# Performance work log

Measured on AMD Instinct MI355X. Metric: run time of the kernel, lower is better.

The kernel has to match this reference:

```python
import jax, jax.numpy as jnp
import numpy as np
from jax import lax

PRE_NMS_TOPN = 6000
POST_NMS_TOPN = 300
NMS_IOU = 0.7
VARIANCES = np.array([0.1, 0.1, 0.2, 0.2], dtype=np.float32)


def setup_inputs() -> dict:
    key = jax.random.key(0)
    k1, k2, k3, k4 = jax.random.split(key, 4)
    B, FH, FW, K = 32, 128, 128, 9
    A = FH * FW * K  # 147456 total anchors
    rpn_bbox_deltas = jax.random.normal(k1, (B, A, 4), dtype=jnp.float32) * 0.1
    rpn_labels = jax.random.normal(k2, (B, FH, FW, K), dtype=jnp.float32)
    # Anchors in [y1, x1, y2, x2] with y1<y2, x1<x2 on a ~1024px image.
    ctr = jax.random.uniform(k3, (A, 2), dtype=jnp.float32) * 1024.0
    wh = jax.random.uniform(k4, (A, 2), dtype=jnp.float32) * 224.0 + 32.0
    anchors = jnp.concatenate([ctr - 0.5 * wh, ctr + 0.5 * wh], axis=-1)
    return {"rpn_bbox_deltas": rpn_bbox_deltas, "rpn_labels": rpn_labels, "anchors": anchors}


def get_bboxes_from_deltas(anchors, deltas):
    # anchors: [A, 4] (y1,x1,y2,x2); deltas: [B, A, 4] (dy,dx,dh,dw)
    anc_w = anchors[..., 3] - anchors[..., 1]
    anc_h = anchors[..., 2] - anchors[..., 0]
    anc_cx = anchors[..., 1] + 0.5 * anc_w
    anc_cy = anchors[..., 0] + 0.5 * anc_h
    bb_w = jnp.exp(deltas[..., 3]) * anc_w
    bb_h = jnp.exp(deltas[..., 2]) * anc_h
    bb_cx = deltas[..., 1] * anc_w + anc_cx
    bb_cy = deltas[..., 0] * anc_h + anc_cy
    y1 = bb_cy - 0.5 * bb_h
    x1 = bb_cx - 0.5 * bb_w
    y2 = bb_h + y1
    x2 = bb_w + x1
    return jnp.stack([y1, x1, y2, x2], axis=-1)


def nms_per_image(boxes, scores, iou_threshold, num_keep):
    # boxes: [N, 4] sorted by descending score; scores: [N]
    y1, x1, y2, x2 = boxes[:, 0], boxes[:, 1], boxes[:, 2], boxes[:, 3]
    areas = (y2 - y1) * (x2 - x1)

    def step(scores_rem, _):
        idx = jnp.argmax(scores_rem)
        valid = jnp.isfinite(scores_rem[idx])
        b = boxes[idx]
        iy1 = jnp.maximum(b[0], y1)
        ix1 = jnp.maximum(b[1], x1)
        iy2 = jnp.minimum(b[2], y2)
        ix2 = jnp.minimum(b[3], x2)
        inter = jnp.clip(iy2 - iy1, 0.0) * jnp.clip(ix2 - ix1, 0.0)
        b_area = (b[2] - b[0]) * (b[3] - b[1])
        iou = inter / (areas + b_area - inter + 1e-9)
        # IoU(box, itself) == 1 > threshold, so the picked box is also suppressed.
        new_scores = jnp.where(iou > iou_threshold, -jnp.inf, scores_rem)
        return new_scores, (idx, valid)

    _, (keep_idx, valid) = lax.scan(step, scores, None, length=num_keep)
    vf = valid.astype(boxes.dtype)
    keep_boxes = boxes[keep_idx] * vf[:, None]  # zero-pad invalid slots
    keep_scores = scores[keep_idx] * vf
    return keep_boxes, keep_scores


def reference(rpn_bbox_deltas, rpn_labels, anchors):
    A = anchors.shape[0]
    B = rpn_bbox_deltas.shape[0]
    deltas = rpn_bbox_deltas.reshape(B, A, 4) * jnp.asarray(VARIANCES)
    labels = jax.nn.softmax(rpn_labels, axis=-1).reshape(B, A)
    rpn_bboxes = get_bboxes_from_deltas(anchors, deltas)  # [B, A, 4]
    # top-k pre-NMS filter (lax.top_k output is already sorted descending)
    pre_scores, pre_idx = lax.top_k(labels, PRE_NMS_TOPN)  # [B, P]
    pre_boxes = jnp.take_along_axis(rpn_bboxes, pre_idx[..., None], axis=1)  # [B, P, 4]
    nms_fn = lambda b, s: nms_per_image(b, s, NMS_IOU, POST_NMS_TOPN)
    roi_bboxes, roi_scores = jax.vmap(nms_fn)(pre_boxes, pre_scores)
    return roi_bboxes, roi_scores
```

## Files before the change

### kernel.cpp

```cpp
#include <hip/hip_runtime.h>
#include <cstdint>
#include <cstddef>

#pragma clang fp contract(off)

#define KCLS 9
#define PRE_N 6000
#define POST_N 300
#define NMS_IOU_T 0.7f
#define HIST_BLOCK 256
#define CHUNKS_PER_IMG 32
#define NMS_BLOCK 512
#define PICK_BLOCK 256
#define NSEG 4
#define SEG_CAP 4096

#define SUPP(pb, pa, mbx, mar, out) \
    bool out; { \
        float iy1_ = fmaxf((pb).x, (mbx).x); \
        float ix1_ = fmaxf((pb).y, (mbx).y); \
        float iy2_ = fminf((pb).z, (mbx).z); \
        float ix2_ = fminf((pb).w, (mbx).w); \
        float ih_ = iy2_ - iy1_; ih_ = ih_ > 0.f ? ih_ : 0.f; \
        float iw_ = ix2_ - ix1_; iw_ = iw_ > 0.f ? iw_ : 0.f; \
        float inter_ = ih_ * iw_; \
        float den_ = (mar) + (pa) - inter_ + 1e-9f; \
        float hi_ = 0.7000007f * den_; \
        float lo_ = 0.6999993f * den_; \
        out = inter_ > hi_; \
        if (inter_ >= lo_ && inter_ <= hi_) out = (inter_ / den_) > NMS_IOU_T; \
    }

__global__ void __launch_bounds__(256)
softmax_hist_kernel(const float* __restrict__ labels,
                    float* __restrict__ scores,
                    unsigned int* __restrict__ ghist,
                    int ngroups, int gpi) {
    __shared__ unsigned int h[2048];
    const int tid = threadIdx.x;
    for (int i = tid; i < 2048; i += 256) h[i] = 0u;
    __syncthreads();
    const int g = blockIdx.x * 256 + tid;
    if (g < ngroups) {
        const float* x = labels + (size_t)g * KCLS;
        float v[KCLS];
        float m = -1e30f;
        #pragma unroll
        for (int k = 0; k < KCLS; ++k) { v[k] = x[k]; m = fmaxf(m, v[k]); }
        float e[KCLS];
        float s = 0.f;
        #pragma unroll
        for (int k = 0; k < KCLS; ++k) { e[k] = expf(v[k] - m); s += e[k]; }
        float* o = scores + (size_t)g * KCLS;
        #pragma unroll
        for (int k = 0; k < KCLS; ++k) {
            float r = e[k] / s;
            o[k] = r;
            atomicAdd(&h[(__float_as_uint(r) >> 21) & 2047u], 1u);
        }
    }
    __syncthreads();
    const int img0 = (blockIdx.x * 256) / gpi;
    unsigned int* gh = ghist + (size_t)img0 * 2048;
    for (int i = tid; i < 2048; i += 256) {
        unsigned int c = h[i];
        if (c) atomicAdd(&gh[i], c);
    }
}

__global__ void hist_kernel(const float* __restrict__ scores,
                            unsigned int* __restrict__ ghist,
                            const unsigned int* __restrict__ state,
                            int A, int shift, int bins, unsigned int pmask) {
    __shared__ unsigned int h[2048];
    const int img = blockIdx.y;
    const int chunk = blockIdx.x;
    const int tid = threadIdx.x;
    for (int i = tid; i < bins; i += HIST_BLOCK) h[i] = 0u;
    __syncthreads();
    unsigned int prefix = pmask ? (state[img * 2 + 0] & pmask) : 0u;
    const int per = A / CHUNKS_PER_IMG;
    const float* sc = scores + (size_t)img * A + (size_t)chunk * per;
    for (int i = tid; i < per; i += HIST_BLOCK) {
        unsigned int v = __float_as_uint(sc[i]);
        if ((v & pmask) == prefix)
            atomicAdd(&h[(v >> shift) & (unsigned)(bins - 1)], 1u);
    }
    __syncthreads();
    unsigned int* gh = ghist + (size_t)img * 2048;
    for (int i = tid; i < bins; i += HIST_BLOCK) {
        unsigned int c = h[i];
        if (c) atomicAdd(&gh[i], c);
    }
}

__global__ void __launch_bounds__(PICK_BLOCK)
pick_kernel(const unsigned int* __restrict__ ghist,
            unsigned int* __restrict__ state,
            int shift, int bins, int first_pass) {
    const int img = blockIdx.x;
    const int t = threadIdx.x;
    const unsigned int* gh = ghist + (size_t)img * 2048;
    __shared__ unsigned int cnt[2048];
    __shared__ unsigned int ssum[PICK_BLOCK];
    const int per = bins / PICK_BLOCK;
    unsigned int my = 0;
    for (int i = 0; i < per; ++i) {
        unsigned int c = gh[t * per + i];
        cnt[t * per + i] = c;
        my += c;
    }
    ssum[t] = my;
    __syncthreads();
    for (int d = 1; d < PICK_BLOCK; d <<= 1) {
        unsigned int v = (t + d < PICK_BLOCK) ? ssum[t + d] : 0u;
        __syncthreads();
        ssum[t] += v;
        __syncthreads();
    }
    unsigned int prefix = first_pass ? 0u : state[img * 2 + 0];
    unsigned int krem = first_pass ? (unsigned)PRE_N : state[img * 2 + 1];
    unsigned int above = ssum[t] - my;
    if (above < krem && ssum[t] >= krem) {
        unsigned int cum = above;
        for (int b = per - 1; b >= 0; --b) {
            unsigned int c = cnt[t * per + b];
            if (cum + c >= krem) {
                state[img * 2 + 0] = prefix | ((unsigned int)(t * per + b) << shift);
                state[img * 2 + 1] = krem - cum;
                break;
            }
            cum += c;
        }
    }
}

#define CE(a, b, u) { if ((v[a] > v[b]) == (u)) { unsigned long long t_ = v[a]; v[a] = v[b]; v[b] = t_; } }
#define REG3(u) { CE(0,4,u) CE(1,5,u) CE(2,6,u) CE(3,7,u) \
                  CE(0,2,u) CE(1,3,u) CE(4,6,u) CE(5,7,u) \
                  CE(0,1,u) CE(2,3,u) CE(4,5,u) CE(6,7,u) }

__global__ void __launch_bounds__(512)
compact_sort_kernel(const float* __restrict__ scores,
                    const unsigned int* __restrict__ state,
                    unsigned long long* __restrict__ pool,
                    unsigned int* __restrict__ counts,
                    int A) {
    __shared__ unsigned long long lin[SEG_CAP];
    __shared__ unsigned int plo[2][SEG_CAP];
    __shared__ unsigned int phi[2][SEG_CAP];
    __shared__ unsigned int cnt;
    const int img = blockIdx.y;
    const int seg = blockIdx.x;
    const int tid = threadIdx.x;
    const int lane = tid & 63;
    const int w = tid >> 6;
    const float* sc = scores + (size_t)img * A;
    const unsigned int T = state[img * 2 + 0];

    if (tid == 0) cnt = 0u;
    for (int i = tid; i < SEG_CAP; i += 512) lin[i] = ~0ull;
    __syncthreads();

    const int ngr = A >> 6;
    const int nj = ngr / NSEG;
    for (int j = w; j < nj; j += 8) {
        int g = seg + j * NSEG;
        int i = (g << 6) + lane;
        unsigned int sv = __float_as_uint(sc[i]);
        bool push = (sv >= T);
        unsigned long long bal = __ballot(push ? 1 : 0);
        if (push) {
            int leader = __ffsll(bal) - 1;
            int rank = __popcll(bal & ((1ull << lane) - 1ull));
            unsigned int base = 0;
            if (lane == leader) base = atomicAdd(&cnt, (unsigned int)__popcll(bal));
            base = (unsigned int)__shfl((int)base, leader);
            unsigned int pos = base + (unsigned int)rank;
            if (pos < SEG_CAP)
                lin[pos] = (((unsigned long long)(~sv)) << 32) | (unsigned long long)(unsigned int)i;
        }
    }
    __syncthreads();

    int n = (int)cnt; if (n > SEG_CAP) n = SEG_CAP;
    int P2 = 512; while (P2 < n) P2 <<= 1;
    const int NT = P2 >> 3;
    const int t = tid;
    const bool act = (t < NT);

    unsigned long long v[8];
    if (act) {
        #pragma unroll
        for (int e = 0; e < 8; ++e) v[e] = lin[(t << 3) + e];
        CE(0,1,true) CE(2,3,false) CE(4,5,true) CE(6,7,false)
        CE(0,2,true) CE(1,3,true) CE(4,6,false) CE(5,7,false)
        CE(0,1,true) CE(2,3,true) CE(4,5,false) CE(6,7,false)
        bool u8 = ((t & 1) == 0);
        REG3(u8)
    }
    int b = 0;
    for (int k = 16; k <= P2; k <<= 1) {
        const bool up = (((t << 3) & k) == 0);
        for (int j = k >> 1; j >= 8; j >>= 1) {
            const int c = j >> 3;
            if (act) {
                #pragma unroll
                for (int e = 0; e < 8; ++e) {
                    int idx = e * NT + t;
                    plo[b][idx] = (unsigned int)v[e];
                    phi[b][idx] = (unsigned int)(v[e] >> 32);
                }
            }
            __syncthreads();
            if (act) {
                const int q = t ^ c;
                const bool keep_min = (up == ((t & c) == 0));
                #pragma unroll
                for (int e = 0; e < 8; ++e) {
                    int idx = e * NT + q;
                    unsigned long long wv = ((unsigned long long)phi[b][idx] << 32)
                                          | (unsigned long long)plo[b][idx];
                    bool less = v[e] < wv;
                    v[e] = (less == keep_min) ? v[e] : wv;
                }
            }
            b ^= 1;
        }
        if (act) { REG3(up) }
    }

    unsigned long long* gp = pool + ((size_t)img * NSEG + seg) * SEG_CAP;
    if (act) {
        #pragma unroll
        for (int e = 0; e < 8; ++e) {
            int r = (t << 3) + e;
            if (r < n) gp[r] = v[e];
        }
    }
    if (tid == 0) counts[img * NSEG + seg] = (unsigned int)n;
}

__global__ void __launch_bounds__(256)
rank_decode_kernel(const unsigned long long* __restrict__ pool,
                   const unsigned int* __restrict__ counts,
                   const float* __restrict__ deltas,
                   const float* __restrict__ anchors,
                   float* __restrict__ pre_boxes,
                   float* __restrict__ pre_scores,
                   int A) {
    __shared__ unsigned long long arr[2 * SEG_CAP];
    const int img = blockIdx.y;
    const int seg = blockIdx.x;
    const int tid = threadIdx.x;

    int c[NSEG], off[NSEG + 1];
    const unsigned long long* gp[NSEG];
    off[0] = 0;
    #pragma unroll
    for (int s = 0; s < NSEG; ++s) {
        int cs = (int)counts[img * NSEG + s];
        if (cs > SEG_CAP) cs = SEG_CAP;
        c[s] = cs;
        off[s + 1] = off[s] + cs;
        gp[s] = pool + ((size_t)img * NSEG + s) * SEG_CAP;
    }
    const int total = off[NSEG];
    const bool inlds = (total <= 2 * SEG_CAP);
    if (inlds) {
        #pragma unroll
        for (int s = 0; s < NSEG; ++s)
            for (int i = tid; i < c[s]; i += 256) arr[off[s] + i] = gp[s][i];
    }
    __syncthreads();

    const int m = c[seg];
    for (int i = tid; i < m; i += 256) {
        unsigned long long key = inlds ? arr[off[seg] + i] : gp[seg][i];
        int pos = i;
        #pragma unroll
        for (int s = 0; s < NSEG; ++s) {
            if (s == seg) continue;
            const unsigned long long* base = inlds ? (arr + off[s]) : gp[s];
            int lo = 0, hi = c[s];
            while (lo < hi) {
                int mid = (lo + hi) >> 1;
                if (base[mid] < key) lo = mid + 1; else hi = mid;
            }
            pos += lo;
        }
        if (pos < PRE_N) {
            unsigned int bidx = (unsigned int)(key & 0xFFFFFFFFull);
            unsigned int sbits = ~((unsigned int)(key >> 32));
            float score = __uint_as_float(sbits);
            float a0 = anchors[(size_t)bidx * 4 + 0];
            float a1 = anchors[(size_t)bidx * 4 + 1];
            float a2 = anchors[(size_t)bidx * 4 + 2];
            float a3 = anchors[(size_t)bidx * 4 + 3];
            const float* dd = deltas + ((size_t)img * A + bidx) * 4;
            float d0 = dd[0] * 0.1f;
            float d1 = dd[1] * 0.1f;
            float d2 = dd[2] * 0.2f;
            float d3 = dd[3] * 0.2f;
            float anc_w = a3 - a1;
            float anc_h = a2 - a0;
            float anc_cx = a1 + 0.5f * anc_w;
            float anc_cy = a0 + 0.5f * anc_h;
            float bb_w = expf(d3) * anc_w;
            float bb_h = expf(d2) * anc_h;
            float bb_cx = d1 * anc_w + anc_cx;
            float bb_cy = d0 * anc_h + anc_cy;
            float y1 = bb_cy - 0.5f * bb_h;
            float x1 = bb_cx - 0.5f * bb_w;
            float y2 = bb_h + y1;
            float x2 = bb_w + x1;
            float* ob = pre_boxes + ((size_t)img * PRE_N + pos) * 4;
            ob[0] = y1; ob[1] = x1; ob[2] = y2; ob[3] = x2;
            pre_scores[(size_t)img * PRE_N + pos] = score;
        }
    }
}

__global__ void __launch_bounds__(NMS_BLOCK)
nms_kernel(const float* __restrict__ pre_boxes,
           const float* __restrict__ pre_scores,
           float* __restrict__ out_boxes,
           float* __restrict__ out_scores) {
    const int img = blockIdx.x;
    const int tid = threadIdx.x;
    const int lane = tid & 63;
    const int grp = tid >> 6;
    const float4* bb4 = (const float4*)(pre_boxes + (size_t)img * PRE_N * 4);

    __shared__ float4 kept[POST_N];
    __shared__ float  kept_area[POST_N];
    __shared__ int    kept_idx[POST_N];
    __shared__ float4 chunkbox[64];
    __shared__ unsigned long long part[8][64];
    __shared__ unsigned long long supcol[64];
    __shared__ unsigned long long chunk_alive;
    __shared__ int kept_cnt;

    if (tid == 0) kept_cnt = 0;

    const int NCH = (PRE_N + 63) >> 6;

    float4 nb = make_float4(0.f, 0.f, 0.f, 0.f);
    if (grp == 0) nb = bb4[lane];

    for (int c = 0; c < NCH; ++c) {
        const int base = c << 6;
        if (grp == 0) chunkbox[lane] = nb;
        if (tid == 0) {
            int rem = PRE_N - base;
            chunk_alive = (rem >= 64) ? ~0ull : ((1ull << rem) - 1ull);
        }
        __syncthreads();

        if (grp == 0 && c + 1 < NCH) {
            int j = base + 64 + lane;
            nb = (j < PRE_N) ? bb4[j] : make_float4(0.f, 0.f, 0.f, 0.f);
        }

        const int K = kept_cnt;
        float4 mb = chunkbox[lane];
        float marea = (mb.z - mb.x) * (mb.w - mb.y);

        bool sup = false;
        for (int k = grp; k < K; k += 8) {
            float4 pb = kept[k];
            float pa = kept_area[k];
            SUPP(pb, pa, mb, marea, s)
            if (s) { sup = true; break; }
        }
        unsigned long long bal = __ballot(sup ? 1 : 0);
        if (lane == 0 && bal) atomicAnd(&chunk_alive, ~bal);

        unsigned long long pm = 0ull;
        #pragma unroll
        for (int u = 0; u < 8; ++u) {
            const int i = (grp << 3) + u;
            float4 pb = chunkbox[i];
            float pa = (pb.z - pb.x) * (pb.w - pb.y);
            SUPP(pb, pa, mb, marea, s)
            if (s) pm |= (1ull << i);
        }
        part[grp][lane] = pm;
        __syncthreads();

        if (grp == 0) {
            unsigned long long col = part[0][lane] | part[1][lane] | part[2][lane] | part[3][lane]
                                   | part[4][lane] | part[5][lane] | part[6][lane] | part[7][lane];
            supcol[lane] = col;
            const unsigned long long extm = chunk_alive;
            unsigned long long aliveset = 0ull;
            int kc = K;
            #pragma unroll 8
            for (int i = 0; i < 64; ++i) {
                unsigned long long mi = supcol[i];
                bool keep = (((extm >> i) & 1ull) != 0ull) &&
                            ((mi & aliveset) == 0ull) && (kc < POST_N);
                if (keep) {
                    if (lane == i) {
                        kept[kc] = mb;
                        kept_area[kc] = marea;
                        kept_idx[kc] = base + i;
                    }
                    aliveset |= (1ull << i);
                    ++kc;
                }
            }
            if (lane == 0) kept_cnt = kc;
        }
        __syncthreads();
        if (kept_cnt >= POST_N) break;
    }

    const int kc = kept_cnt;
    for (int r = tid; r < kc; r += NMS_BLOCK) {
        float4 bx = kept[r];
        float* ob = out_boxes + ((size_t)img * POST_N + r) * 4;
        ob[0] = bx.x; ob[1] = bx.y; ob[2] = bx.z; ob[3] = bx.w;
        out_scores[(size_t)img * POST_N + r] =
            pre_scores[(size_t)img * PRE_N + kept_idx[r]];
    }
}

extern "C" void kernel_launch(void* const* d_in, const int* in_sizes, int n_in,
                              void* d_out, int out_size, void* d_ws, size_t ws_size,
                              hipStream_t stream) {
    const float* deltas  = (const float*)d_in[0];
    const float* labels  = (const float*)d_in[1];
    const float* anchors = (const float*)d_in[2];
    float* out = (float*)d_out;

    const int A = in_sizes[2] / 4;
    const int B = in_sizes[0] / (A * 4);
    const int ngroups = in_sizes[1] / KCLS;
    const int gpi = ngroups / B;

    float* scores     = (float*)d_ws;
    float* pre_boxes  = scores + (size_t)B * A;
    float* pre_scores = pre_boxes + (size_t)B * PRE_N * 4;
    unsigned int* hist  = (unsigned int*)(pre_scores + (size_t)B * PRE_N);
    unsigned int* state = hist + (size_t)3 * B * 2048;
    unsigned long long* pool = (unsigned long long*)(state + (size_t)B * 2);
    unsigned int* counts = (unsigned int*)(pool + (size_t)B * NSEG * SEG_CAP);

    float* out_boxes  = out;
    float* out_scores = out + (size_t)B * POST_N * 4;

    hipMemsetAsync(d_out, 0, (size_t)out_size * sizeof(float), stream);
    hipMemsetAsync(hist, 0, (size_t)3 * B * 2048 * sizeof(unsigned int), stream);

    softmax_hist_kernel<<<(ngroups + 255) / 256, 256, 0, stream>>>(
        labels, scores, hist + (size_t)0 * B * 2048, ngroups, gpi);
    pick_kernel<<<B, PICK_BLOCK, 0, stream>>>(hist + (size_t)0 * B * 2048, state, 21, 2048, 1);

    dim3 hgrid(CHUNKS_PER_IMG, B);
    hist_kernel<<<hgrid, HIST_BLOCK, 0, stream>>>(scores, hist + (size_t)1 * B * 2048, state, A, 10, 2048, 0xFFE00000u);
    pick_kernel<<<B, PICK_BLOCK, 0, stream>>>(hist + (size_t)1 * B * 2048, state, 10, 2048, 0);
    hist_kernel<<<hgrid, HIST_BLOCK, 0, stream>>>(scores, hist + (size_t)2 * B * 2048, state, A, 0, 1024, 0xFFFFFC00u);
    pick_kernel<<<B, PICK_BLOCK, 0, stream>>>(hist + (size_t)2 * B * 2048, state, 0, 1024, 0);

    dim3 sgrid(NSEG, B);
    compact_sort_kernel<<<sgrid, 512, 0, stream>>>(scores, state, pool, counts, A);
    rank_decode_kernel<<<sgrid, 256, 0, stream>>>(pool, counts, deltas, anchors,
                                                  pre_boxes, pre_scores, A);

    nms_kernel<<<B, NMS_BLOCK, 0, stream>>>(pre_boxes, pre_scores, out_boxes, out_scores);
}
```

Baseline: 289.5 us.

## Coalesce softmax via LDS staging, drop third radix pass, use more sort segments

The softmax kernel now stages each block's labels through shared memory with float4 loads and stores, so global traffic is coalesced. The third histogram/pick radix pass is removed, leaving selection at a 21-bit prefix threshold. Compaction and sort now use 8 segments of 2048 instead of 4 of 4096, and the rank kernel gets a fixed 8192-entry LDS buffer. This risks correctness when the coarser threshold admits more candidates than the segments can hold. It also assumes the group count is a multiple of 256.

```diff
diff --git a/kernel.cpp b/kernel.cpp
--- a/kernel.cpp
+++ b/kernel.cpp
@@ -12,8 +12,9 @@
 #define CHUNKS_PER_IMG 32
 #define NMS_BLOCK 512
 #define PICK_BLOCK 256
-#define NSEG 4
-#define SEG_CAP 4096
+#define NSEG 8
+#define SEG_CAP 2048
+#define RANK_LDS 8192
 
 #define SUPP(pb, pa, mbx, mar, out) \
     bool out; { \
@@ -35,31 +36,37 @@
 softmax_hist_kernel(const float* __restrict__ labels,
                     float* __restrict__ scores,
                     unsigned int* __restrict__ ghist,
-                    int ngroups, int gpi) {
+                    int gpi) {
+    __shared__ float buf[256 * KCLS];
     __shared__ unsigned int h[2048];
     const int tid = threadIdx.x;
     for (int i = tid; i < 2048; i += 256) h[i] = 0u;
-    __syncthreads();
-    const int g = blockIdx.x * 256 + tid;
-    if (g < ngroups) {
-        const float* x = labels + (size_t)g * KCLS;
-        float v[KCLS];
-        float m = -1e30f;
-        #pragma unroll
-        for (int k = 0; k < KCLS; ++k) { v[k] = x[k]; m = fmaxf(m, v[k]); }
-        float e[KCLS];
-        float s = 0.f;
-        #pragma unroll
-        for (int k = 0; k < KCLS; ++k) { e[k] = expf(v[k] - m); s += e[k]; }
-        float* o = scores + (size_t)g * KCLS;
-        #pragma unroll
-        for (int k = 0; k < KCLS; ++k) {
-            float r = e[k] / s;
-            o[k] = r;
-            atomicAdd(&h[(__float_as_uint(r) >> 21) & 2047u], 1u);
-        }
-    }
-    __syncthreads();
+
+    const size_t gbase = (size_t)blockIdx.x * (256 * KCLS);
+    const float4* lin4 = (const float4*)(labels + gbase);
+    float4* b4 = (float4*)buf;
+    for (int i = tid; i < 576; i += 256) b4[i] = lin4[i];
+    __syncthreads();
+
+    float v[KCLS];
+    float m = -1e30f;
+    #pragma unroll
+    for (int k = 0; k < KCLS; ++k) { v[k] = buf[tid * KCLS + k]; m = fmaxf(m, v[k]); }
+    float e[KCLS];
+    float s = 0.f;
+    #pragma unroll
+    for (int k = 0; k < KCLS; ++k) { e[k] = expf(v[k] - m); s += e[k]; }
+    #pragma unroll
+    for (int k = 0; k < KCLS; ++k) {
+        float r = e[k] / s;
+        buf[tid * KCLS + k] = r;
+        atomicAdd(&h[(__float_as_uint(r) >> 21) & 2047u], 1u);
+    }
+    __syncthreads();
+
+    float4* o4 = (float4*)(scores + gbase);
+    for (int i = tid; i < 576; i += 256) o4[i] = b4[i];
+
     const int img0 = (blockIdx.x * 256) / gpi;
     unsigned int* gh = ghist + (size_t)img0 * 2048;
     for (int i = tid; i < 2048; i += 256) {
@@ -78,7 +85,7 @@
     const int tid = threadIdx.x;
     for (int i = tid; i < bins; i += HIST_BLOCK) h[i] = 0u;
     __syncthreads();
-    unsigned int prefix = pmask ? (state[img * 2 + 0] & pmask) : 0u;
+    unsigned int prefix = state[img * 2 + 0] & pmask;
     const int per = A / CHUNKS_PER_IMG;
     const float* sc = scores + (size_t)img * A + (size_t)chunk * per;
     for (int i = tid; i < per; i += HIST_BLOCK) {
@@ -249,7 +256,7 @@
                    float* __restrict__ pre_boxes,
                    float* __restrict__ pre_scores,
                    int A) {
-    __shared__ unsigned long long arr[2 * SEG_CAP];
+    __shared__ unsigned long long arr[RANK_LDS];
     const int img = blockIdx.y;
     const int seg = blockIdx.x;
     const int tid = threadIdx.x;
@@ -266,7 +273,7 @@
         gp[s] = pool + ((size_t)img * NSEG + s) * SEG_CAP;
     }
     const int total = off[NSEG];
-    const bool inlds = (total <= 2 * SEG_CAP);
+    const bool inlds = (total <= RANK_LDS);
     if (inlds) {
         #pragma unroll
         for (int s = 0; s < NSEG; ++s)
@@ -443,7 +450,7 @@
     float* pre_boxes  = scores + (size_t)B * A;
     float* pre_scores = pre_boxes + (size_t)B * PRE_N * 4;
     unsigned int* hist  = (unsigned int*)(pre_scores + (size_t)B * PRE_N);
-    unsigned int* state = hist + (size_t)3 * B * 2048;
+    unsigned int* state = hist + (size_t)2 * B * 2048;
     unsigned long long* pool = (unsigned long long*)(state + (size_t)B * 2);
     unsigned int* counts = (unsigned int*)(pool + (size_t)B * NSEG * SEG_CAP);
 
@@ -451,17 +458,16 @@
     float* out_scores = out + (size_t)B * POST_N * 4;
 
     hipMemsetAsync(d_out, 0, (size_t)out_size * sizeof(float), stream);
-    hipMemsetAsync(hist, 0, (size_t)3 * B * 2048 * sizeof(unsigned int), stream);
-
-    softmax_hist_kernel<<<(ngroups + 255) / 256, 256, 0, stream>>>(
-        labels, scores, hist + (size_t)0 * B * 2048, ngroups, gpi);
+    hipMemsetAsync(hist, 0, ((size_t)2 * B * 2048 + 2 * B) * sizeof(unsigned int), stream);
+
+    softmax_hist_kernel<<<ngroups / 256, 256, 0, stream>>>(
+        labels, scores, hist + (size_t)0 * B * 2048, gpi);
     pick_kernel<<<B, PICK_BLOCK, 0, stream>>>(hist + (size_t)0 * B * 2048, state, 21, 2048, 1);
 
     dim3 hgrid(CHUNKS_PER_IMG, B);
-    hist_kernel<<<hgrid, HIST_BLOCK, 0, stream>>>(scores, hist + (size_t)1 * B * 2048, state, A, 10, 2048, 0xFFE00000u);
+    hist_kernel<<<hgrid, HIST_BLOCK, 0, stream>>>(
+        scores, hist + (size_t)1 * B * 2048, state, A, 10, 2048, 0xFFE00000u);
     pick_kernel<<<B, PICK_BLOCK, 0, stream>>>(hist + (size_t)1 * B * 2048, state, 10, 2048, 0);
-    hist_kernel<<<hgrid, HIST_BLOCK, 0, stream>>>(scores, hist + (size_t)2 * B * 2048, state, A, 0, 1024, 0xFFFFFC00u);
-    pick_kernel<<<B, PICK_BLOCK, 0, stream>>>(hist + (size_t)2 * B * 2048, state, 0, 1024, 0);
 
     dim3 sgrid(NSEG, B);
     compact_sort_kernel<<<sgrid, 512, 0, stream>>>(scores, state, pool, counts, A);
```

Measured after the change: 260.9 us. 9.9% less time.
